# Kernel optimization log

Hardware: AMD Instinct MI355X
Metric: run time of the kernel (lower is better)

## Reference

```python
import jax, jax.numpy as jnp
import numpy as np


def setup_inputs() -> dict:
    key = jax.random.key(0)
    k1, k2, k3 = jax.random.split(key, 3)
    B, M, J = 4096, 64, 24  # batch, n_max_markers, n_joints
    points = jax.random.normal(k1, (B, M, 3), dtype=jnp.float32)
    weight = jax.random.uniform(k2, (B, M, J), dtype=jnp.float32)  # positive soft weights
    offset = jax.random.normal(k3, (B, M, J, 3), dtype=jnp.float32)
    return {"points": points, "weight": weight, "offset": offset}


def reference(points, weight, offset):
    # P: per-joint marker offsets (B, J, 3, M); Q: world marker positions (B, 1, 3, M)
    P = jnp.transpose(offset, (0, 2, 3, 1))
    Q = jnp.transpose(points, (0, 2, 1))[:, None]
    w = jnp.transpose(weight, (0, 2, 1))[:, :, None]  # (B, J, 1, M)

    wsum = jnp.sum(w, axis=-1)                   # (B, J, 1)
    P_ = jnp.sum(P * w, axis=-1) / wsum          # (B, J, 3) weighted centroid of offsets
    Q_ = jnp.sum(Q * w, axis=-1) / wsum          # (B, J, 3) weighted centroid of markers

    X = P - P_[..., None]                        # (B, J, 3, M)
    Y = Q - Q_[..., None]                        # (B, J, 3, M) via broadcast

    # Cross-covariance S = X @ Y^T (NOTE: original multiplies un-weighted centered coords)
    S = jnp.einsum('bjdm,bjem->bjde', X, Y)      # (B, J, 3, 3)

    U, _, Vh = jnp.linalg.svd(S)
    V = jnp.swapaxes(Vh, -1, -2)
    Ut = jnp.swapaxes(U, -1, -2)
    det = jnp.linalg.det(jnp.matmul(V, Ut))      # (B, J) reflection correction
    Ut = Ut.at[..., -1, :].multiply(det[..., None])
    R = jnp.matmul(V, Ut)                        # (B, J, 3, 3) optimal rotation
    t = Q_[..., None] - jnp.matmul(R, P_[..., None])  # (B, J, 3, 1)
    return R, t
```

## Files before the change

kernel.cpp:

```cpp
#include <hip/hip_runtime.h>


constexpr int M = 64;
constexpr int J = 24;
constexpr int NACC = 22;
constexpr int NWS  = 15;
constexpr int KSP  = 8;
constexpr int SPW  = 8;
constexpr int SPB  = 32;

__global__ __launch_bounds__(256, 6) void accum_kernel(
    const float* __restrict__ points,
    const float* __restrict__ weight,
    const float* __restrict__ offset,
    float* __restrict__ ws,
    int bj_total)
{
    const int t    = threadIdx.x;
    const int lane = t & 63;
    const int wv   = t >> 6;
    const int k    = lane >> 3;
    const int sl   = lane & 7;
    const int bj   = blockIdx.x * SPB + wv * SPW + sl;
    const int bjc  = bj < bj_total ? bj : bj_total - 1;
    const int b    = bjc / J;
    const int j    = bjc - b * J;

    const float* wq = weight + (size_t)b * (M * J) + (size_t)(k * 8) * J + j;
    const float* oq = offset + ((size_t)b * (M * J) + (size_t)(k * 8) * J + j) * 3;
    const float* pq = points + (size_t)b * (M * 3) + (size_t)(k * 8) * 3;

    float acc[NACC];
#pragma unroll
    for (int n = 0; n < NACC; ++n) acc[n] = 0.0f;

#pragma unroll
    for (int i = 0; i < M / KSP; ++i) {
        float w  = wq[i * J];
        float o0 = oq[i * (J * 3) + 0];
        float o1 = oq[i * (J * 3) + 1];
        float o2 = oq[i * (J * 3) + 2];
        float p0 = pq[i * 3 + 0];
        float p1 = pq[i * 3 + 1];
        float p2 = pq[i * 3 + 2];
        acc[0] += w;
        acc[1] = fmaf(w, o0, acc[1]);  acc[2] = fmaf(w, o1, acc[2]);  acc[3] = fmaf(w, o2, acc[3]);
        acc[4] = fmaf(w, p0, acc[4]);  acc[5] = fmaf(w, p1, acc[5]);  acc[6] = fmaf(w, p2, acc[6]);
        acc[7] += o0; acc[8] += o1; acc[9] += o2;
        acc[10] += p0; acc[11] += p1; acc[12] += p2;
        acc[13] = fmaf(o0, p0, acc[13]); acc[14] = fmaf(o0, p1, acc[14]); acc[15] = fmaf(o0, p2, acc[15]);
        acc[16] = fmaf(o1, p0, acc[16]); acc[17] = fmaf(o1, p1, acc[17]); acc[18] = fmaf(o1, p2, acc[18]);
        acc[19] = fmaf(o2, p0, acc[19]); acc[20] = fmaf(o2, p1, acc[20]); acc[21] = fmaf(o2, p2, acc[21]);
    }

#pragma unroll
    for (int n = 0; n < NACC; ++n) {
        float v = acc[n];
        v += __shfl_xor(v, 8);
        v += __shfl_xor(v, 16);
        v += __shfl_xor(v, 32);
        acc[n] = v;
    }

    if (k != 0 || bj >= bj_total) return;

    const float inv = __builtin_amdgcn_rcpf(acc[0]);
    const float cP0 = acc[1] * inv, cP1 = acc[2] * inv, cP2 = acc[3] * inv;
    const float cQ0 = acc[4] * inv, cQ1 = acc[5] * inv, cQ2 = acc[6] * inv;
    const float To0 = acc[7], To1 = acc[8], To2 = acc[9];
    const float Tp0 = acc[10], Tp1 = acc[11], Tp2 = acc[12];
    const float fM = (float)M;
    float Sv[NWS];
    Sv[0] = acc[13] - cP0 * Tp0 - cQ0 * To0 + fM * cP0 * cQ0;
    Sv[1] = acc[14] - cP0 * Tp1 - cQ1 * To0 + fM * cP0 * cQ1;
    Sv[2] = acc[15] - cP0 * Tp2 - cQ2 * To0 + fM * cP0 * cQ2;
    Sv[3] = acc[16] - cP1 * Tp0 - cQ0 * To1 + fM * cP1 * cQ0;
    Sv[4] = acc[17] - cP1 * Tp1 - cQ1 * To1 + fM * cP1 * cQ1;
    Sv[5] = acc[18] - cP1 * Tp2 - cQ2 * To1 + fM * cP1 * cQ2;
    Sv[6] = acc[19] - cP2 * Tp0 - cQ0 * To2 + fM * cP2 * cQ0;
    Sv[7] = acc[20] - cP2 * Tp1 - cQ1 * To2 + fM * cP2 * cQ1;
    Sv[8] = acc[21] - cP2 * Tp2 - cQ2 * To2 + fM * cP2 * cQ2;
    Sv[9]  = cP0; Sv[10] = cP1; Sv[11] = cP2;
    Sv[12] = cQ0; Sv[13] = cQ1; Sv[14] = cQ2;
#pragma unroll
    for (int n = 0; n < NWS; ++n) ws[(size_t)n * bj_total + bj] = Sv[n];
}

template<int P, int Q>
__device__ __forceinline__ void jrot(float A[4][4], float V[4][4]) {
    float apq = A[P][Q];
    float theta = (A[Q][Q] - A[P][P]) * __builtin_amdgcn_rcpf(2.0f * apq);
    float t = __builtin_amdgcn_rcpf(fabsf(theta) + __builtin_amdgcn_sqrtf(fmaf(theta, theta, 1.0f)));
    t = (theta < 0.0f) ? -t : t;
    t = (apq == 0.0f) ? 0.0f : t;
    float c = __builtin_amdgcn_rsqf(fmaf(t, t, 1.0f));
    float s = t * c;
#pragma unroll
    for (int k = 0; k < 4; ++k) {
        float akp = A[k][P], akq = A[k][Q];
        A[k][P] = c * akp - s * akq;
        A[k][Q] = s * akp + c * akq;
    }
#pragma unroll
    for (int k = 0; k < 4; ++k) {
        float apk = A[P][k], aqk = A[Q][k];
        A[P][k] = c * apk - s * aqk;
        A[Q][k] = s * apk + c * aqk;
        float vkp = V[k][P], vkq = V[k][Q];
        V[k][P] = c * vkp - s * vkq;
        V[k][Q] = s * vkp + c * vkq;
    }
}

__device__ __forceinline__ void horn_solve(
    float S00, float S01, float S02, float S10, float S11, float S12,
    float S20, float S21, float S22,
    float cP0, float cP1, float cP2, float cQ0, float cQ1, float cQ2,
    float* __restrict__ Rout, float* __restrict__ tout)
{
    float A[4][4], V[4][4];
    A[0][0] = S00 + S11 + S22;
    A[0][1] = A[1][0] = S12 - S21;
    A[0][2] = A[2][0] = S20 - S02;
    A[0][3] = A[3][0] = S01 - S10;
    A[1][1] = S00 - S11 - S22;
    A[1][2] = A[2][1] = S01 + S10;
    A[1][3] = A[3][1] = S02 + S20;
    A[2][2] = -S00 + S11 - S22;
    A[2][3] = A[3][2] = S12 + S21;
    A[3][3] = -S00 - S11 + S22;
#pragma unroll
    for (int r = 0; r < 4; ++r)
#pragma unroll
        for (int c = 0; c < 4; ++c)
            V[r][c] = (r == c) ? 1.0f : 0.0f;

#pragma unroll 1
    for (int sweep = 0; sweep < 6; ++sweep) {
        jrot<0, 1>(A, V); jrot<0, 2>(A, V); jrot<0, 3>(A, V);
        jrot<1, 2>(A, V); jrot<1, 3>(A, V); jrot<2, 3>(A, V);
    }

    float best = A[0][0];
    float qw = V[0][0], qx = V[1][0], qy = V[2][0], qz = V[3][0];
#pragma unroll
    for (int i = 1; i < 4; ++i) {
        bool better = A[i][i] > best;
        best = better ? A[i][i] : best;
        qw = better ? V[0][i] : qw;
        qx = better ? V[1][i] : qx;
        qy = better ? V[2][i] : qy;
        qz = better ? V[3][i] : qz;
    }
    float nrm = __builtin_amdgcn_rsqf(qw * qw + qx * qx + qy * qy + qz * qz);
    qw *= nrm; qx *= nrm; qy *= nrm; qz *= nrm;

    float R00 = 1.f - 2.f * (qy * qy + qz * qz);
    float R01 = 2.f * (qx * qy - qw * qz);
    float R02 = 2.f * (qx * qz + qw * qy);
    float R10 = 2.f * (qx * qy + qw * qz);
    float R11 = 1.f - 2.f * (qx * qx + qz * qz);
    float R12 = 2.f * (qy * qz - qw * qx);
    float R20 = 2.f * (qx * qz - qw * qy);
    float R21 = 2.f * (qy * qz + qw * qx);
    float R22 = 1.f - 2.f * (qx * qx + qy * qy);

    Rout[0] = R00; Rout[1] = R01; Rout[2] = R02;
    Rout[3] = R10; Rout[4] = R11; Rout[5] = R12;
    Rout[6] = R20; Rout[7] = R21; Rout[8] = R22;
    tout[0] = cQ0 - (R00 * cP0 + R01 * cP1 + R02 * cP2);
    tout[1] = cQ1 - (R10 * cP0 + R11 * cP1 + R12 * cP2);
    tout[2] = cQ2 - (R20 * cP0 + R21 * cP1 + R22 * cP2);
}

__global__ __launch_bounds__(64) void solve_kernel(
    const float* __restrict__ ws, float* __restrict__ out, int bj_total)
{
    int tid = blockIdx.x * 64 + threadIdx.x;
    if (tid >= bj_total) return;
    float Sv[NWS];
#pragma unroll
    for (int n = 0; n < NWS; ++n) Sv[n] = ws[(size_t)n * bj_total + tid];
    float Rr[9], tr[3];
    horn_solve(Sv[0], Sv[1], Sv[2], Sv[3], Sv[4], Sv[5], Sv[6], Sv[7], Sv[8],
               Sv[9], Sv[10], Sv[11], Sv[12], Sv[13], Sv[14], Rr, tr);
    float* Rout = out + (size_t)tid * 9;
#pragma unroll
    for (int n = 0; n < 9; ++n) Rout[n] = Rr[n];
    float* tout = out + (size_t)bj_total * 9 + (size_t)tid * 3;
    tout[0] = tr[0]; tout[1] = tr[1]; tout[2] = tr[2];
}

__global__ __launch_bounds__(256) void fused_kernel(
    const float* __restrict__ points, const float* __restrict__ weight,
    const float* __restrict__ offset, float* __restrict__ out, int bj_total)
{
    int tid = blockIdx.x * blockDim.x + threadIdx.x;
    if (tid >= bj_total) return;
    int b = tid / J, j = tid - b * J;
    const float* wq = weight + (size_t)b * M * J + j;
    const float* oq = offset + ((size_t)b * M * J + j) * 3;
    const float* pq = points + (size_t)b * M * 3;
    float a[NACC];
#pragma unroll
    for (int n = 0; n < NACC; ++n) a[n] = 0.0f;
#pragma unroll 4
    for (int m = 0; m < M; ++m) {
        float w = wq[m * J];
        float o0 = oq[m * (J * 3) + 0], o1 = oq[m * (J * 3) + 1], o2 = oq[m * (J * 3) + 2];
        float p0 = pq[m * 3 + 0], p1 = pq[m * 3 + 1], p2 = pq[m * 3 + 2];
        a[0] += w;
        a[1] = fmaf(w, o0, a[1]); a[2] = fmaf(w, o1, a[2]); a[3] = fmaf(w, o2, a[3]);
        a[4] = fmaf(w, p0, a[4]); a[5] = fmaf(w, p1, a[5]); a[6] = fmaf(w, p2, a[6]);
        a[7] += o0; a[8] += o1; a[9] += o2;
        a[10] += p0; a[11] += p1; a[12] += p2;
        a[13] = fmaf(o0, p0, a[13]); a[14] = fmaf(o0, p1, a[14]); a[15] = fmaf(o0, p2, a[15]);
        a[16] = fmaf(o1, p0, a[16]); a[17] = fmaf(o1, p1, a[17]); a[18] = fmaf(o1, p2, a[18]);
        a[19] = fmaf(o2, p0, a[19]); a[20] = fmaf(o2, p1, a[20]); a[21] = fmaf(o2, p2, a[21]);
    }
    float inv = __builtin_amdgcn_rcpf(a[0]);
    float cP0 = a[1] * inv, cP1 = a[2] * inv, cP2 = a[3] * inv;
    float cQ0 = a[4] * inv, cQ1 = a[5] * inv, cQ2 = a[6] * inv;
    const float fM = (float)M;
    float S00 = a[13] - cP0 * a[10] - cQ0 * a[7] + fM * cP0 * cQ0;
    float S01 = a[14] - cP0 * a[11] - cQ1 * a[7] + fM * cP0 * cQ1;
    float S02 = a[15] - cP0 * a[12] - cQ2 * a[7] + fM * cP0 * cQ2;
    float S10 = a[16] - cP1 * a[10] - cQ0 * a[8] + fM * cP1 * cQ0;
    float S11 = a[17] - cP1 * a[11] - cQ1 * a[8] + fM * cP1 * cQ1;
    float S12 = a[18] - cP1 * a[12] - cQ2 * a[8] + fM * cP1 * cQ2;
    float S20 = a[19] - cP2 * a[10] - cQ0 * a[9] + fM * cP2 * cQ0;
    float S21 = a[20] - cP2 * a[11] - cQ1 * a[9] + fM * cP2 * cQ1;
    float S22 = a[21] - cP2 * a[12] - cQ2 * a[9] + fM * cP2 * cQ2;
    float Rr[9], tr[3];
    horn_solve(S00, S01, S02, S10, S11, S12, S20, S21, S22,
               cP0, cP1, cP2, cQ0, cQ1, cQ2, Rr, tr);
    float* Rout = out + (size_t)tid * 9;
#pragma unroll
    for (int n = 0; n < 9; ++n) Rout[n] = Rr[n];
    float* tout = out + (size_t)bj_total * 9 + (size_t)tid * 3;
    tout[0] = tr[0]; tout[1] = tr[1]; tout[2] = tr[2];
}

extern "C" void kernel_launch(void* const* d_in, const int* in_sizes, int n_in,
                              void* d_out, int out_size, void* d_ws, size_t ws_size,
                              hipStream_t stream) {
    const float* points = (const float*)d_in[0];
    const float* weight = (const float*)d_in[1];
    const float* offset = (const float*)d_in[2];
    float* out = (float*)d_out;

    int B = in_sizes[0] / (M * 3);
    int bj_total = B * J;

    size_t need = (size_t)NWS * bj_total * sizeof(float);
    if (ws_size >= need) {
        int grid1 = (bj_total + SPB - 1) / SPB;
        accum_kernel<<<grid1, 256, 0, stream>>>(points, weight, offset, (float*)d_ws, bj_total);
        solve_kernel<<<(bj_total + 63) / 64, 64, 0, stream>>>((const float*)d_ws, out, bj_total);
    } else {
        fused_kernel<<<(bj_total + 255) / 256, 256, 0, stream>>>(points, weight, offset, out, bj_total);
    }
}
```

Measured before the change: 146.6 us.

## Process four joints per thread with float4 loads and AoS workspace

The accumulation kernel now gives each thread four consecutive joints, so weights and offsets are fetched as float4 vectors and the point loads and point sums are shared across those joints. The workspace switches from a struct-of-arrays layout with 15 fields to a padded 16-float record per joint, letting both kernels read and write it with float4 accesses. The solve kernel moves to 256-thread blocks. In exchange the accumulation kernel holds many more registers (76 accumulators), and its occupancy hint is lowered accordingly.

```diff
diff --git a/kernel.cpp b/kernel.cpp
--- a/kernel.cpp
+++ b/kernel.cpp
@@ -3,87 +3,116 @@
 
 constexpr int M = 64;
 constexpr int J = 24;
-constexpr int NACC = 22;
-constexpr int NWS  = 15;
-constexpr int KSP  = 8;
-constexpr int SPW  = 8;
-constexpr int SPB  = 32;
-
-__global__ __launch_bounds__(256, 6) void accum_kernel(
+constexpr int NQ = J / 4;
+constexpr int KSP = 8;
+constexpr int QPW = 8;
+constexpr int QPB = 32;
+
+__global__ __launch_bounds__(256, 3) void accum_kernel(
     const float* __restrict__ points,
     const float* __restrict__ weight,
     const float* __restrict__ offset,
     float* __restrict__ ws,
-    int bj_total)
+    int q4_total, int bj_total)
 {
     const int t    = threadIdx.x;
     const int lane = t & 63;
     const int wv   = t >> 6;
     const int k    = lane >> 3;
     const int sl   = lane & 7;
-    const int bj   = blockIdx.x * SPB + wv * SPW + sl;
-    const int bjc  = bj < bj_total ? bj : bj_total - 1;
-    const int b    = bjc / J;
-    const int j    = bjc - b * J;
-
-    const float* wq = weight + (size_t)b * (M * J) + (size_t)(k * 8) * J + j;
-    const float* oq = offset + ((size_t)b * (M * J) + (size_t)(k * 8) * J + j) * 3;
-    const float* pq = points + (size_t)b * (M * 3) + (size_t)(k * 8) * 3;
-
-    float acc[NACC];
-#pragma unroll
-    for (int n = 0; n < NACC; ++n) acc[n] = 0.0f;
+    const int q4   = blockIdx.x * QPB + wv * QPW + sl;
+    const int q4c  = q4 < q4_total ? q4 : q4_total - 1;
+    const int b    = q4c / NQ;
+    const int jg   = q4c - b * NQ;
+    const int j0   = jg * 4;
+
+    const float4* wq = (const float4*)(weight + (size_t)b * (M * J) + (size_t)(k * 8) * J + j0);
+    const float4* oq = (const float4*)(offset + ((size_t)b * (M * J) + (size_t)(k * 8) * J + j0) * 3);
+    const float*  pq = points + (size_t)b * (M * 3) + (size_t)(k * 8) * 3;
+
+    float a[4][19];
+    float tp[3] = {0.f, 0.f, 0.f};
+#pragma unroll
+    for (int jj = 0; jj < 4; ++jj)
+#pragma unroll
+        for (int n = 0; n < 19; ++n) a[jj][n] = 0.0f;
 
 #pragma unroll
     for (int i = 0; i < M / KSP; ++i) {
-        float w  = wq[i * J];
-        float o0 = oq[i * (J * 3) + 0];
-        float o1 = oq[i * (J * 3) + 1];
-        float o2 = oq[i * (J * 3) + 2];
+        float4 wf = wq[i * (J / 4)];
+        float4 oa = oq[i * (J * 3 / 4) + 0];
+        float4 ob = oq[i * (J * 3 / 4) + 1];
+        float4 oc = oq[i * (J * 3 / 4) + 2];
         float p0 = pq[i * 3 + 0];
         float p1 = pq[i * 3 + 1];
         float p2 = pq[i * 3 + 2];
-        acc[0] += w;
-        acc[1] = fmaf(w, o0, acc[1]);  acc[2] = fmaf(w, o1, acc[2]);  acc[3] = fmaf(w, o2, acc[3]);
-        acc[4] = fmaf(w, p0, acc[4]);  acc[5] = fmaf(w, p1, acc[5]);  acc[6] = fmaf(w, p2, acc[6]);
-        acc[7] += o0; acc[8] += o1; acc[9] += o2;
-        acc[10] += p0; acc[11] += p1; acc[12] += p2;
-        acc[13] = fmaf(o0, p0, acc[13]); acc[14] = fmaf(o0, p1, acc[14]); acc[15] = fmaf(o0, p2, acc[15]);
-        acc[16] = fmaf(o1, p0, acc[16]); acc[17] = fmaf(o1, p1, acc[17]); acc[18] = fmaf(o1, p2, acc[18]);
-        acc[19] = fmaf(o2, p0, acc[19]); acc[20] = fmaf(o2, p1, acc[20]); acc[21] = fmaf(o2, p2, acc[21]);
-    }
-
-#pragma unroll
-    for (int n = 0; n < NACC; ++n) {
-        float v = acc[n];
+        tp[0] += p0; tp[1] += p1; tp[2] += p2;
+        float of[12];
+        of[0] = oa.x; of[1]  = oa.y; of[2]  = oa.z; of[3]  = oa.w;
+        of[4] = ob.x; of[5]  = ob.y; of[6]  = ob.z; of[7]  = ob.w;
+        of[8] = oc.x; of[9]  = oc.y; of[10] = oc.z; of[11] = oc.w;
+        float wf4[4];
+        wf4[0] = wf.x; wf4[1] = wf.y; wf4[2] = wf.z; wf4[3] = wf.w;
+#pragma unroll
+        for (int jj = 0; jj < 4; ++jj) {
+            float w  = wf4[jj];
+            float o0 = of[jj * 3 + 0];
+            float o1 = of[jj * 3 + 1];
+            float o2 = of[jj * 3 + 2];
+            a[jj][0] += w;
+            a[jj][1] = fmaf(w, o0, a[jj][1]);  a[jj][2] = fmaf(w, o1, a[jj][2]);  a[jj][3] = fmaf(w, o2, a[jj][3]);
+            a[jj][4] = fmaf(w, p0, a[jj][4]);  a[jj][5] = fmaf(w, p1, a[jj][5]);  a[jj][6] = fmaf(w, p2, a[jj][6]);
+            a[jj][7] += o0; a[jj][8] += o1; a[jj][9] += o2;
+            a[jj][10] = fmaf(o0, p0, a[jj][10]); a[jj][11] = fmaf(o0, p1, a[jj][11]); a[jj][12] = fmaf(o0, p2, a[jj][12]);
+            a[jj][13] = fmaf(o1, p0, a[jj][13]); a[jj][14] = fmaf(o1, p1, a[jj][14]); a[jj][15] = fmaf(o1, p2, a[jj][15]);
+            a[jj][16] = fmaf(o2, p0, a[jj][16]); a[jj][17] = fmaf(o2, p1, a[jj][17]); a[jj][18] = fmaf(o2, p2, a[jj][18]);
+        }
+    }
+
+#pragma unroll
+    for (int jj = 0; jj < 4; ++jj)
+#pragma unroll
+        for (int n = 0; n < 19; ++n) {
+            float v = a[jj][n];
+            v += __shfl_xor(v, 8);
+            v += __shfl_xor(v, 16);
+            v += __shfl_xor(v, 32);
+            a[jj][n] = v;
+        }
+#pragma unroll
+    for (int n = 0; n < 3; ++n) {
+        float v = tp[n];
         v += __shfl_xor(v, 8);
         v += __shfl_xor(v, 16);
         v += __shfl_xor(v, 32);
-        acc[n] = v;
-    }
-
-    if (k != 0 || bj >= bj_total) return;
-
-    const float inv = __builtin_amdgcn_rcpf(acc[0]);
-    const float cP0 = acc[1] * inv, cP1 = acc[2] * inv, cP2 = acc[3] * inv;
-    const float cQ0 = acc[4] * inv, cQ1 = acc[5] * inv, cQ2 = acc[6] * inv;
-    const float To0 = acc[7], To1 = acc[8], To2 = acc[9];
-    const float Tp0 = acc[10], Tp1 = acc[11], Tp2 = acc[12];
+        tp[n] = v;
+    }
+
+    if (k != 0 || q4 >= q4_total) return;
+
     const float fM = (float)M;
-    float Sv[NWS];
-    Sv[0] = acc[13] - cP0 * Tp0 - cQ0 * To0 + fM * cP0 * cQ0;
-    Sv[1] = acc[14] - cP0 * Tp1 - cQ1 * To0 + fM * cP0 * cQ1;
-    Sv[2] = acc[15] - cP0 * Tp2 - cQ2 * To0 + fM * cP0 * cQ2;
-    Sv[3] = acc[16] - cP1 * Tp0 - cQ0 * To1 + fM * cP1 * cQ0;
-    Sv[4] = acc[17] - cP1 * Tp1 - cQ1 * To1 + fM * cP1 * cQ1;
-    Sv[5] = acc[18] - cP1 * Tp2 - cQ2 * To1 + fM * cP1 * cQ2;
-    Sv[6] = acc[19] - cP2 * Tp0 - cQ0 * To2 + fM * cP2 * cQ0;
-    Sv[7] = acc[20] - cP2 * Tp1 - cQ1 * To2 + fM * cP2 * cQ1;
-    Sv[8] = acc[21] - cP2 * Tp2 - cQ2 * To2 + fM * cP2 * cQ2;
-    Sv[9]  = cP0; Sv[10] = cP1; Sv[11] = cP2;
-    Sv[12] = cQ0; Sv[13] = cQ1; Sv[14] = cQ2;
-#pragma unroll
-    for (int n = 0; n < NWS; ++n) ws[(size_t)n * bj_total + bj] = Sv[n];
+#pragma unroll
+    for (int jj = 0; jj < 4; ++jj) {
+        const float inv = __builtin_amdgcn_rcpf(a[jj][0]);
+        const float cP0 = a[jj][1] * inv, cP1 = a[jj][2] * inv, cP2 = a[jj][3] * inv;
+        const float cQ0 = a[jj][4] * inv, cQ1 = a[jj][5] * inv, cQ2 = a[jj][6] * inv;
+        const float To0 = a[jj][7], To1 = a[jj][8], To2 = a[jj][9];
+        float4 f0, f1, f2, f3;
+        f0.x = a[jj][10] - cP0 * tp[0] - cQ0 * To0 + fM * cP0 * cQ0;
+        f0.y = a[jj][11] - cP0 * tp[1] - cQ1 * To0 + fM * cP0 * cQ1;
+        f0.z = a[jj][12] - cP0 * tp[2] - cQ2 * To0 + fM * cP0 * cQ2;
+        f0.w = a[jj][13] - cP1 * tp[0] - cQ0 * To1 + fM * cP1 * cQ0;
+        f1.x = a[jj][14] - cP1 * tp[1] - cQ1 * To1 + fM * cP1 * cQ1;
+        f1.y = a[jj][15] - cP1 * tp[2] - cQ2 * To1 + fM * cP1 * cQ2;
+        f1.z = a[jj][16] - cP2 * tp[0] - cQ0 * To2 + fM * cP2 * cQ0;
+        f1.w = a[jj][17] - cP2 * tp[1] - cQ1 * To2 + fM * cP2 * cQ1;
+        f2.x = a[jj][18] - cP2 * tp[2] - cQ2 * To2 + fM * cP2 * cQ2;
+        f2.y = cP0; f2.z = cP1; f2.w = cP2;
+        f3.x = cQ0; f3.y = cQ1; f3.z = cQ2; f3.w = 0.0f;
+        const int bj = (b * NQ + jg) * 4 + jj;
+        float4* dst = (float4*)(ws + (size_t)bj * 16);
+        dst[0] = f0; dst[1] = f1; dst[2] = f2; dst[3] = f3;
+    }
 }
 
 template<int P, int Q>
@@ -173,17 +202,16 @@
     tout[2] = cQ2 - (R20 * cP0 + R21 * cP1 + R22 * cP2);
 }
 
-__global__ __launch_bounds__(64) void solve_kernel(
+__global__ __launch_bounds__(256) void solve_kernel(
     const float* __restrict__ ws, float* __restrict__ out, int bj_total)
 {
-    int tid = blockIdx.x * 64 + threadIdx.x;
+    int tid = blockIdx.x * 256 + threadIdx.x;
     if (tid >= bj_total) return;
-    float Sv[NWS];
-#pragma unroll
-    for (int n = 0; n < NWS; ++n) Sv[n] = ws[(size_t)n * bj_total + tid];
+    const float4* v = (const float4*)(ws + (size_t)tid * 16);
+    float4 f0 = v[0], f1 = v[1], f2 = v[2], f3 = v[3];
     float Rr[9], tr[3];
-    horn_solve(Sv[0], Sv[1], Sv[2], Sv[3], Sv[4], Sv[5], Sv[6], Sv[7], Sv[8],
-               Sv[9], Sv[10], Sv[11], Sv[12], Sv[13], Sv[14], Rr, tr);
+    horn_solve(f0.x, f0.y, f0.z, f0.w, f1.x, f1.y, f1.z, f1.w, f2.x,
+               f2.y, f2.z, f2.w, f3.x, f3.y, f3.z, Rr, tr);
     float* Rout = out + (size_t)tid * 9;
 #pragma unroll
     for (int n = 0; n < 9; ++n) Rout[n] = Rr[n];
@@ -201,9 +229,9 @@
     const float* wq = weight + (size_t)b * M * J + j;
     const float* oq = offset + ((size_t)b * M * J + j) * 3;
     const float* pq = points + (size_t)b * M * 3;
-    float a[NACC];
-#pragma unroll
-    for (int n = 0; n < NACC; ++n) a[n] = 0.0f;
+    float a[22];
+#pragma unroll
+    for (int n = 0; n < 22; ++n) a[n] = 0.0f;
 #pragma unroll 4
     for (int m = 0; m < M; ++m) {
         float w = wq[m * J];
@@ -251,12 +279,14 @@
 
     int B = in_sizes[0] / (M * 3);
     int bj_total = B * J;
-
-    size_t need = (size_t)NWS * bj_total * sizeof(float);
+    int q4_total = B * NQ;
+
+    size_t need = (size_t)bj_total * 16 * sizeof(float);
     if (ws_size >= need) {
-        int grid1 = (bj_total + SPB - 1) / SPB;
-        accum_kernel<<<grid1, 256, 0, stream>>>(points, weight, offset, (float*)d_ws, bj_total);
-        solve_kernel<<<(bj_total + 63) / 64, 64, 0, stream>>>((const float*)d_ws, out, bj_total);
+        int grid1 = (q4_total + QPB - 1) / QPB;
+        accum_kernel<<<grid1, 256, 0, stream>>>(points, weight, offset, (float*)d_ws,
+                                                q4_total, bj_total);
+        solve_kernel<<<(bj_total + 255) / 256, 256, 0, stream>>>((const float*)d_ws, out, bj_total);
     } else {
         fused_kernel<<<(bj_total + 255) / 256, 256, 0, stream>>>(points, weight, offset, out, bj_total);
     }
```

Result: slower. 156.5 us (+6.7%).

## Stage per-batch inputs in LDS with float4 loads and pack workspace as float4

Applied to the files above, without the earlier changes.

The accumulation kernel now runs one block per batch element and copies that element's weights, offsets and points into shared memory with coalesced float4 loads. Each joint is then reduced by 8 lanes reading from LDS, with the loop start rotated per lane to reduce bank conflicts. This replaces the earlier strided global gathers. The workspace moves from a structure-of-arrays layout to 16-float records per joint, written and read as float4, and the solve kernel now uses 256-thread blocks. The cost is 25KB of LDS per block, which caps occupancy, and a quarter of each block's threads sit idle after the load phase.

```diff
diff --git a/kernel.cpp b/kernel.cpp
--- a/kernel.cpp
+++ b/kernel.cpp
@@ -4,45 +4,60 @@
 constexpr int M = 64;
 constexpr int J = 24;
 constexpr int NACC = 22;
-constexpr int NWS  = 15;
-constexpr int KSP  = 8;
-constexpr int SPW  = 8;
-constexpr int SPB  = 32;
-
-__global__ __launch_bounds__(256, 6) void accum_kernel(
+
+constexpr int LW = 0;
+constexpr int LO = 1536;
+constexpr int LP = 6144;
+constexpr int LTOT = 6336;
+
+__global__ __launch_bounds__(256) void accum_kernel(
     const float* __restrict__ points,
     const float* __restrict__ weight,
     const float* __restrict__ offset,
     float* __restrict__ ws,
     int bj_total)
 {
-    const int t    = threadIdx.x;
-    const int lane = t & 63;
-    const int wv   = t >> 6;
-    const int k    = lane >> 3;
-    const int sl   = lane & 7;
-    const int bj   = blockIdx.x * SPB + wv * SPW + sl;
-    const int bjc  = bj < bj_total ? bj : bj_total - 1;
-    const int b    = bjc / J;
-    const int j    = bjc - b * J;
-
-    const float* wq = weight + (size_t)b * (M * J) + (size_t)(k * 8) * J + j;
-    const float* oq = offset + ((size_t)b * (M * J) + (size_t)(k * 8) * J + j) * 3;
-    const float* pq = points + (size_t)b * (M * 3) + (size_t)(k * 8) * 3;
+    __shared__ float smem[LTOT];
+    const int t = threadIdx.x;
+    const int b = blockIdx.x;
+
+    float4* s4 = (float4*)smem;
+    const float4* wg4 = (const float4*)(weight + (size_t)b * (M * J));
+    const float4* og4 = (const float4*)(offset + (size_t)b * (M * J * 3));
+    const float4* pg4 = (const float4*)(points + (size_t)b * (M * 3));
+#pragma unroll
+    for (int i = 0; i < 2; ++i) {
+        int idx = t + i * 256;
+        if (idx < 384) s4[LW / 4 + idx] = wg4[idx];
+    }
+#pragma unroll
+    for (int i = 0; i < 5; ++i) {
+        int idx = t + i * 256;
+        if (idx < 1152) s4[LO / 4 + idx] = og4[idx];
+    }
+    if (t < 48) s4[LP / 4 + t] = pg4[t];
+
+    __syncthreads();
+
+    if (t >= 192) return;
+    const int j = t >> 3;
+    const int k = t & 7;
 
     float acc[NACC];
 #pragma unroll
     for (int n = 0; n < NACC; ++n) acc[n] = 0.0f;
 
 #pragma unroll
-    for (int i = 0; i < M / KSP; ++i) {
-        float w  = wq[i * J];
-        float o0 = oq[i * (J * 3) + 0];
-        float o1 = oq[i * (J * 3) + 1];
-        float o2 = oq[i * (J * 3) + 2];
-        float p0 = pq[i * 3 + 0];
-        float p1 = pq[i * 3 + 1];
-        float p2 = pq[i * 3 + 2];
+    for (int ii = 0; ii < M / 8; ++ii) {
+        const int i = (ii + k) & 7;
+        const int m = k * 8 + i;
+        float w  = smem[LW + m * 24 + j];
+        float o0 = smem[LO + m * 72 + j * 3 + 0];
+        float o1 = smem[LO + m * 72 + j * 3 + 1];
+        float o2 = smem[LO + m * 72 + j * 3 + 2];
+        float p0 = smem[LP + m * 3 + 0];
+        float p1 = smem[LP + m * 3 + 1];
+        float p2 = smem[LP + m * 3 + 2];
         acc[0] += w;
         acc[1] = fmaf(w, o0, acc[1]);  acc[2] = fmaf(w, o1, acc[2]);  acc[3] = fmaf(w, o2, acc[3]);
         acc[4] = fmaf(w, p0, acc[4]);  acc[5] = fmaf(w, p1, acc[5]);  acc[6] = fmaf(w, p2, acc[6]);
@@ -56,13 +71,13 @@
 #pragma unroll
     for (int n = 0; n < NACC; ++n) {
         float v = acc[n];
-        v += __shfl_xor(v, 8);
-        v += __shfl_xor(v, 16);
-        v += __shfl_xor(v, 32);
+        v += __shfl_xor(v, 1);
+        v += __shfl_xor(v, 2);
+        v += __shfl_xor(v, 4);
         acc[n] = v;
     }
 
-    if (k != 0 || bj >= bj_total) return;
+    if (k != 0) return;
 
     const float inv = __builtin_amdgcn_rcpf(acc[0]);
     const float cP0 = acc[1] * inv, cP1 = acc[2] * inv, cP2 = acc[3] * inv;
@@ -70,20 +85,22 @@
     const float To0 = acc[7], To1 = acc[8], To2 = acc[9];
     const float Tp0 = acc[10], Tp1 = acc[11], Tp2 = acc[12];
     const float fM = (float)M;
-    float Sv[NWS];
-    Sv[0] = acc[13] - cP0 * Tp0 - cQ0 * To0 + fM * cP0 * cQ0;
-    Sv[1] = acc[14] - cP0 * Tp1 - cQ1 * To0 + fM * cP0 * cQ1;
-    Sv[2] = acc[15] - cP0 * Tp2 - cQ2 * To0 + fM * cP0 * cQ2;
-    Sv[3] = acc[16] - cP1 * Tp0 - cQ0 * To1 + fM * cP1 * cQ0;
-    Sv[4] = acc[17] - cP1 * Tp1 - cQ1 * To1 + fM * cP1 * cQ1;
-    Sv[5] = acc[18] - cP1 * Tp2 - cQ2 * To1 + fM * cP1 * cQ2;
-    Sv[6] = acc[19] - cP2 * Tp0 - cQ0 * To2 + fM * cP2 * cQ0;
-    Sv[7] = acc[20] - cP2 * Tp1 - cQ1 * To2 + fM * cP2 * cQ1;
-    Sv[8] = acc[21] - cP2 * Tp2 - cQ2 * To2 + fM * cP2 * cQ2;
-    Sv[9]  = cP0; Sv[10] = cP1; Sv[11] = cP2;
-    Sv[12] = cQ0; Sv[13] = cQ1; Sv[14] = cQ2;
-#pragma unroll
-    for (int n = 0; n < NWS; ++n) ws[(size_t)n * bj_total + bj] = Sv[n];
+    float4 f0, f1, f2, f3;
+    f0.x = acc[13] - cP0 * Tp0 - cQ0 * To0 + fM * cP0 * cQ0;
+    f0.y = acc[14] - cP0 * Tp1 - cQ1 * To0 + fM * cP0 * cQ1;
+    f0.z = acc[15] - cP0 * Tp2 - cQ2 * To0 + fM * cP0 * cQ2;
+    f0.w = acc[16] - cP1 * Tp0 - cQ0 * To1 + fM * cP1 * cQ0;
+    f1.x = acc[17] - cP1 * Tp1 - cQ1 * To1 + fM * cP1 * cQ1;
+    f1.y = acc[18] - cP1 * Tp2 - cQ2 * To1 + fM * cP1 * cQ2;
+    f1.z = acc[19] - cP2 * Tp0 - cQ0 * To2 + fM * cP2 * cQ0;
+    f1.w = acc[20] - cP2 * Tp1 - cQ1 * To2 + fM * cP2 * cQ1;
+    f2.x = acc[21] - cP2 * Tp2 - cQ2 * To2 + fM * cP2 * cQ2;
+    f2.y = cP0; f2.z = cP1; f2.w = cP2;
+    f3.x = cQ0; f3.y = cQ1; f3.z = cQ2; f3.w = 0.0f;
+
+    const int bj = b * J + j;
+    float4* dst = (float4*)(ws + (size_t)bj * 16);
+    dst[0] = f0; dst[1] = f1; dst[2] = f2; dst[3] = f3;
 }
 
 template<int P, int Q>
@@ -173,17 +190,16 @@
     tout[2] = cQ2 - (R20 * cP0 + R21 * cP1 + R22 * cP2);
 }
 
-__global__ __launch_bounds__(64) void solve_kernel(
+__global__ __launch_bounds__(256) void solve_kernel(
     const float* __restrict__ ws, float* __restrict__ out, int bj_total)
 {
-    int tid = blockIdx.x * 64 + threadIdx.x;
+    int tid = blockIdx.x * 256 + threadIdx.x;
     if (tid >= bj_total) return;
-    float Sv[NWS];
-#pragma unroll
-    for (int n = 0; n < NWS; ++n) Sv[n] = ws[(size_t)n * bj_total + tid];
+    const float4* v = (const float4*)(ws + (size_t)tid * 16);
+    float4 f0 = v[0], f1 = v[1], f2 = v[2], f3 = v[3];
     float Rr[9], tr[3];
-    horn_solve(Sv[0], Sv[1], Sv[2], Sv[3], Sv[4], Sv[5], Sv[6], Sv[7], Sv[8],
-               Sv[9], Sv[10], Sv[11], Sv[12], Sv[13], Sv[14], Rr, tr);
+    horn_solve(f0.x, f0.y, f0.z, f0.w, f1.x, f1.y, f1.z, f1.w, f2.x,
+               f2.y, f2.z, f2.w, f3.x, f3.y, f3.z, Rr, tr);
     float* Rout = out + (size_t)tid * 9;
 #pragma unroll
     for (int n = 0; n < 9; ++n) Rout[n] = Rr[n];
@@ -252,11 +268,10 @@
     int B = in_sizes[0] / (M * 3);
     int bj_total = B * J;
 
-    size_t need = (size_t)NWS * bj_total * sizeof(float);
+    size_t need = (size_t)bj_total * 16 * sizeof(float);
     if (ws_size >= need) {
-        int grid1 = (bj_total + SPB - 1) / SPB;
-        accum_kernel<<<grid1, 256, 0, stream>>>(points, weight, offset, (float*)d_ws, bj_total);
-        solve_kernel<<<(bj_total + 63) / 64, 64, 0, stream>>>((const float*)d_ws, out, bj_total);
+        accum_kernel<<<B, 256, 0, stream>>>(points, weight, offset, (float*)d_ws, bj_total);
+        solve_kernel<<<(bj_total + 255) / 256, 256, 0, stream>>>((const float*)d_ws, out, bj_total);
     } else {
         fused_kernel<<<(bj_total + 255) / 256, 256, 0, stream>>>(points, weight, offset, out, bj_total);
     }
```

Measured after the change: 151.0 us. 1.03x slower.
